# Optimization experiments

Hardware: AMD Instinct MI355X
Metric: run time of the kernel (lower is better)

The kernel has to match this reference:

```python
import jax, jax.numpy as jnp
import numpy as np

S, B, H = 2048, 2, 1024
NH = 16
HD = H // NH  # 64


def setup_inputs() -> dict:
    key = jax.random.key(0)
    k1, k2 = jax.random.split(key)
    hidden_states = jax.random.normal(k1, (S, B, H), dtype=jnp.float32)
    W_qkv = jax.random.normal(k2, (3 * H, H), dtype=jnp.float32) * (H ** -0.5)
    b_qkv = jnp.zeros((3 * H,), dtype=jnp.float32)
    return {"hidden_states": hidden_states, "W_qkv": W_qkv, "b_qkv": b_qkv}


def reference(hidden_states, W_qkv, b_qkv):
    s, b, h = hidden_states.shape
    # QKV projection: [S,B,3H] -> [S,B,NH,3*HD] -> split
    qkv = hidden_states @ W_qkv.T + b_qkv
    qkv = qkv.reshape(s, b, NH, 3 * HD)
    q, k, v = jnp.split(qkv, 3, axis=-1)  # each [S,B,NH,HD]
    norm_factor = HD ** -0.5
    # scores: [B,NH,Sq,Sk]
    scores = jnp.einsum('sbhd,tbhd->bhst', q, k) * norm_factor
    # Cumsum sequence-op (seq_op_in_fp32=True): cumsum over key dim, scaled by Sq^-0.5
    probs = jnp.cumsum(scores.astype(jnp.float32), axis=-1) * (s ** -0.5)
    probs = probs.astype(hidden_states.dtype)
    # PV: [B,NH,Sq,HD] -> seq-first [Sq,B,NH*HD]
    ctx = jnp.einsum('bhst,tbhd->sbhd', probs, v)
    return ctx.reshape(s, b, h)
```

## Files before the change

kernel.cpp:

```cpp
#include <hip/hip_runtime.h>

#define S 2048
#define B 2
#define H 1024
#define NH 16
#define HD 64
#define THREE_H 3072
#define ROWS (S*B)

typedef __attribute__((ext_vector_type(8))) short short8;
typedef __attribute__((ext_vector_type(4))) float f32x4;
typedef const __attribute__((address_space(1))) unsigned int* gptr_t;
typedef __attribute__((address_space(3))) unsigned int* lptr_t;

#define N8_A (ROWS * H / 8)
#define N8_W (THREE_H * H / 8)

__device__ __forceinline__ ushort f2bf(float f) {
    union { float f; unsigned u; } v; v.f = f;
    unsigned r = v.u + 0x7fffu + ((v.u >> 16) & 1u);
    return (ushort)(r >> 16);
}
__device__ __forceinline__ float bf2f(ushort u) {
    union { unsigned u; float f; } v; v.u = ((unsigned)u) << 16;
    return v.f;
}

__global__ void cast_both(const float* __restrict__ A, const float* __restrict__ W,
                          ushort* __restrict__ Ab, ushort* __restrict__ Wb) {
    int i = blockIdx.x * 256 + threadIdx.x;
    const float4* s4;
    ushort* dst;
    if (i < N8_A) { s4 = (const float4*)A; dst = Ab; }
    else if (i < N8_A + N8_W) { s4 = (const float4*)W; dst = Wb; i -= N8_A; }
    else return;
    float4 a = s4[2 * i], b = s4[2 * i + 1];
    short8 o;
    o[0] = f2bf(a.x); o[1] = f2bf(a.y); o[2] = f2bf(a.z); o[3] = f2bf(a.w);
    o[4] = f2bf(b.x); o[5] = f2bf(b.y); o[6] = f2bf(b.z); o[7] = f2bf(b.w);
    *(short8*)(dst + 8 * (size_t)i) = o;
}

__global__ __launch_bounds__(256) void qkv_gemm_mfma(const ushort* __restrict__ Abf,
                                                     const ushort* __restrict__ Wbf,
                                                     const float* __restrict__ bias,
                                                     ushort* __restrict__ Qb,
                                                     ushort* __restrict__ Kb,
                                                     ushort* __restrict__ Vraw) {
    __shared__ ushort Abuf[128 * 32];
    __shared__ ushort Bbuf[128 * 32];
    const int tid = threadIdx.x;
    const int wave = tid >> 6, lane = tid & 63;
    const int wr = wave >> 1, wc = wave & 1;
    const int row0 = blockIdx.x * 128;
    const int col0 = blockIdx.y * 128;

    f32x4 acc[4][4] = {};

    const int lrow = lane >> 2;
    const int gk = ((lane & 3) ^ (lrow & 3)) * 8;
    const int il = lane & 15, ko = lane >> 4;

    for (int k0 = 0; k0 < H; k0 += 32) {
#pragma unroll
        for (int p = 0; p < 2; ++p) {
            int c = wave * 2 + p;
            int row = c * 16 + lrow;
            __builtin_amdgcn_global_load_lds(
                (gptr_t)&Abf[(size_t)(row0 + row) * H + k0 + gk],
                (lptr_t)&Abuf[c * 512 + lane * 8], 16, 0, 0);
            __builtin_amdgcn_global_load_lds(
                (gptr_t)&Wbf[(size_t)(col0 + row) * H + k0 + gk],
                (lptr_t)&Bbuf[c * 512 + lane * 8], 16, 0, 0);
        }
        __syncthreads();

        short8 af[4], bfr[4];
#pragma unroll
        for (int m = 0; m < 4; ++m) {
            int ar = wr * 64 + m * 16 + il;
            int br = wc * 64 + m * 16 + il;
            af[m]  = *(const short8*)&Abuf[ar * 32 + (ko ^ (ar & 3)) * 8];
            bfr[m] = *(const short8*)&Bbuf[br * 32 + (ko ^ (br & 3)) * 8];
        }
#pragma unroll
        for (int m = 0; m < 4; ++m)
#pragma unroll
            for (int n = 0; n < 4; ++n)
                acc[m][n] = __builtin_amdgcn_mfma_f32_16x16x32_bf16(af[m], bfr[n], acc[m][n], 0, 0, 0);
        __syncthreads();
    }

#pragma unroll
    for (int n = 0; n < 4; ++n) {
        int cbase = col0 + wc * 64 + n * 16;
        int h   = cbase / 192;
        int r3  = cbase % 192;
        int sel = r3 >> 6;
        int d   = (r3 & 63) + il;
        float bv = bias[cbase + il];
        ushort* dst = (sel == 0) ? Qb : (sel == 1) ? Kb : Vraw;
#pragma unroll
        for (int m = 0; m < 4; ++m) {
            int rowb = row0 + wr * 64 + m * 16 + ko * 4;
#pragma unroll
            for (int j = 0; j < 4; ++j) {
                int r = rowb + j;
                int s = r >> 1, b = r & 1;
                dst[((size_t)((b * NH + h) * S + s)) * HD + d] = f2bf(acc[m][n][j] + bv);
            }
        }
    }
}

__global__ __launch_bounds__(256) void ktrans_chunksum(const ushort* __restrict__ Kb,
                                                       ushort* __restrict__ Kt,
                                                       const ushort* __restrict__ Vraw,
                                                       float* __restrict__ csum) {
    __shared__ ushort Ks[64][72];
    const int gb = blockIdx.x;
    const int tid = threadIdx.x;
    if (gb < 1024) {
        const int bh = gb >> 5;
        const int t0 = (gb & 31) * 64;
        {
            const int tt = tid >> 2, part = (tid & 3) * 16;
            const ushort* src = Kb + ((size_t)bh * S + t0 + tt) * HD + part;
            *(short8*)&Ks[tt][part]     = *(const short8*)(src);
            *(short8*)&Ks[tt][part + 8] = *(const short8*)(src + 8);
        }
        __syncthreads();
        {
            const int d = tid >> 2, tq = (tid & 3) * 16;
            ushort tmp[16];
#pragma unroll
            for (int k = 0; k < 16; ++k) tmp[k] = Ks[tq + k][d];
            ushort* dst = Kt + ((size_t)bh * HD + d) * S + t0 + tq;
            short8 o0, o1;
#pragma unroll
            for (int k = 0; k < 8; ++k) { o0[k] = tmp[k]; o1[k] = tmp[8 + k]; }
            *(short8*)dst = o0;
            *(short8*)(dst + 8) = o1;
        }
    } else {
        int idx = (gb - 1024) * 256 + tid;
        int col = idx & 2047;
        int chunk = idx >> 11;
        const ushort* vp = Vraw + ((size_t)(col >> 6) * S + chunk * 32) * HD + (col & 63);
        float s = 0.f;
#pragma unroll
        for (int t = 0; t < 32; ++t) s += bf2f(vp[(size_t)t * HD]);
        csum[chunk * 2048 + col] = s;
    }
}

__global__ void vsuft_final(const ushort* __restrict__ Vraw, const float* __restrict__ csum,
                            ushort* __restrict__ Vt) {
    int idx = blockIdx.x * 256 + threadIdx.x;
    int col = idx & 2047;
    int chunk = idx >> 11;
    int bh = col >> 6, d = col & 63;
    float acc = 0.f;
    for (int c = chunk + 1; c < 64; ++c) acc += csum[c * 2048 + col];
    const ushort* vp = Vraw + ((size_t)bh * S + chunk * 32) * HD + d;
    ushort buf[32];
#pragma unroll
    for (int tt = 31; tt >= 0; --tt) {
        acc += bf2f(vp[(size_t)tt * HD]);
        buf[tt] = f2bf(acc);
    }
    ushort* op = Vt + ((size_t)bh * HD + d) * S + chunk * 32;
#pragma unroll
    for (int q = 0; q < 4; ++q) {
        short8 o;
#pragma unroll
        for (int k = 0; k < 8; ++k) o[k] = buf[q * 8 + k];
        *(short8*)(op + q * 8) = o;
    }
}

__global__ __launch_bounds__(256) void kvm_mfma(const ushort* __restrict__ Kt,
                                                const ushort* __restrict__ Vt,
                                                float* __restrict__ Mpart) {
    __shared__ float red[2][4096];
    const int bh = blockIdx.x, kb = blockIdx.y;
    const int tid = threadIdx.x, wave = tid >> 6, lane = tid & 63;
    const int slice = kb * 4 + wave;
    const ushort* Kp = Kt + (size_t)bh * HD * S;
    const ushort* Vp = Vt + (size_t)bh * HD * S;
    f32x4 acc[4][4] = {};
    const int il = lane & 15, g = lane >> 4;
    const int tbase = slice * 128 + g * 8;
#pragma unroll
    for (int ks = 0; ks < 4; ++ks) {
        const int t = tbase + ks * 32;
        short8 af[4], bfv[4];
#pragma unroll
        for (int m = 0; m < 4; ++m) af[m]  = *(const short8*)&Kp[(size_t)(m * 16 + il) * S + t];
#pragma unroll
        for (int n = 0; n < 4; ++n) bfv[n] = *(const short8*)&Vp[(size_t)(n * 16 + il) * S + t];
#pragma unroll
        for (int m = 0; m < 4; ++m)
#pragma unroll
            for (int n = 0; n < 4; ++n)
                acc[m][n] = __builtin_amdgcn_mfma_f32_16x16x32_bf16(af[m], bfv[n], acc[m][n], 0, 0, 0);
    }
#define DUMP(dstbuf)                                                        \
    { float* _d = (dstbuf);                                                 \
      _Pragma("unroll") for (int m = 0; m < 4; ++m)                         \
      _Pragma("unroll") for (int n = 0; n < 4; ++n)                         \
      _Pragma("unroll") for (int j = 0; j < 4; ++j)                         \
          _d[(m * 16 + g * 4 + j) * 64 + n * 16 + il] = acc[m][n][j]; }
#define ADDIN(srcbuf)                                                       \
    { const float* _s = (srcbuf);                                           \
      _Pragma("unroll") for (int m = 0; m < 4; ++m)                         \
      _Pragma("unroll") for (int n = 0; n < 4; ++n)                         \
      _Pragma("unroll") for (int j = 0; j < 4; ++j)                         \
          acc[m][n][j] += _s[(m * 16 + g * 4 + j) * 64 + n * 16 + il]; }
    if (wave == 1) DUMP(red[0]);
    if (wave == 3) DUMP(red[1]);
    __syncthreads();
    if (wave == 0) ADDIN(red[0]);
    if (wave == 2) ADDIN(red[1]);
    __syncthreads();
    if (wave == 2) DUMP(red[0]);
    __syncthreads();
    if (wave == 0) {
        ADDIN(red[0]);
        float* Mp = Mpart + ((size_t)kb * 32 + bh) * 4096;
#pragma unroll
        for (int m = 0; m < 4; ++m)
#pragma unroll
            for (int n = 0; n < 4; ++n)
#pragma unroll
                for (int j = 0; j < 4; ++j)
                    Mp[(m * 16 + g * 4 + j) * 64 + n * 16 + il] = acc[m][n][j];
    }
#undef DUMP
#undef ADDIN
}

__global__ __launch_bounds__(256) void qm_mfma(const ushort* __restrict__ Qb,
                                               const float* __restrict__ Mpart,
                                               float* __restrict__ out) {
    __shared__ ushort Mt[64][72];
    const int bh = blockIdx.x, b = bh >> 4, h = bh & 15;
    const int tid = threadIdx.x;
    {
        const int i = tid >> 2, jq = (tid & 3) * 16;
        f32x4 s0 = {}, s1 = {}, s2 = {}, s3 = {};
#pragma unroll
        for (int sl = 0; sl < 4; ++sl) {
            const float* p = Mpart + ((size_t)sl * 32 + bh) * 4096 + i * 64 + jq;
            s0 += *(const f32x4*)(p);
            s1 += *(const f32x4*)(p + 4);
            s2 += *(const f32x4*)(p + 8);
            s3 += *(const f32x4*)(p + 12);
        }
#pragma unroll
        for (int k = 0; k < 4; ++k) {
            Mt[jq + 0  + k][i] = f2bf(s0[k]);
            Mt[jq + 4  + k][i] = f2bf(s1[k]);
            Mt[jq + 8  + k][i] = f2bf(s2[k]);
            Mt[jq + 12 + k][i] = f2bf(s3[k]);
        }
    }
    __syncthreads();
    const int wave = tid >> 6, lane = tid & 63;
    const int sl15 = lane & 15, koct = (lane >> 4) * 8;
    const int s0b = blockIdx.y * 256 + wave * 64;
    f32x4 acc[4][4] = {};
#pragma unroll
    for (int ks = 0; ks < 2; ++ks) {
        short8 af[4], bfv[4];
#pragma unroll
        for (int m = 0; m < 4; ++m) {
            int s = s0b + m * 16 + sl15;
            af[m] = *(const short8*)&Qb[((size_t)bh * S + s) * HD + ks * 32 + koct];
        }
#pragma unroll
        for (int n = 0; n < 4; ++n)
            bfv[n] = *(const short8*)&Mt[n * 16 + sl15][ks * 32 + koct];
#pragma unroll
        for (int m = 0; m < 4; ++m)
#pragma unroll
            for (int n = 0; n < 4; ++n)
                acc[m][n] = __builtin_amdgcn_mfma_f32_16x16x32_bf16(af[m], bfv[n], acc[m][n], 0, 0, 0);
    }
    const float scale = 0.125f * 0.02209708691207961f;
#pragma unroll
    for (int m = 0; m < 4; ++m)
#pragma unroll
        for (int n = 0; n < 4; ++n)
#pragma unroll
            for (int j = 0; j < 4; ++j) {
                int s = s0b + m * 16 + (lane >> 4) * 4 + j;
                int d = n * 16 + sl15;
                out[(size_t)(s * B + b) * H + h * 64 + d] = acc[m][n][j] * scale;
            }
}

extern "C" void kernel_launch(void* const* d_in, const int* in_sizes, int n_in,
                              void* d_out, int out_size, void* d_ws, size_t ws_size,
                              hipStream_t stream) {
    const float* hidden = (const float*)d_in[0];
    const float* W      = (const float*)d_in[1];
    const float* bias   = (const float*)d_in[2];
    float* out = (float*)d_out;

    ushort* Qb    = (ushort*)d_ws;
    ushort* Kb    = Qb + 4194304;
    ushort* Kt    = Kb + 4194304;
    ushort* Vraw  = Kt + 4194304;
    ushort* Vt    = Vraw + 4194304;
    float*  csum  = (float*)(Vt + 4194304);
    float*  Mpart = csum + 131072;
    ushort* Abf   = (ushort*)(Mpart + 524288);
    ushort* Wbf   = Abf + 4194304;

    cast_both<<<(N8_A + N8_W + 255) / 256, 256, 0, stream>>>(hidden, W, Abf, Wbf);
    qkv_gemm_mfma<<<dim3(ROWS / 128, THREE_H / 128), 256, 0, stream>>>(Abf, Wbf, bias, Qb, Kb, Vraw);
    ktrans_chunksum<<<1536, 256, 0, stream>>>(Kb, Kt, Vraw, csum);
    vsuft_final<<<512, 256, 0, stream>>>(Vraw, csum, Vt);
    kvm_mfma<<<dim3(32, 4), 256, 0, stream>>>(Kt, Vt, Mpart);
    qm_mfma<<<dim3(32, 8), 256, 0, stream>>>(Qb, Mpart, out);
}
```

Baseline: 78.04 us.

## Write K and V transposed from GEMM epilogue and replace suffix scan with single-pass wave scan

The QKV GEMM epilogue now writes K and V directly in a transposed [bh][d][t] layout, so the separate K-transpose and V chunk-sum kernels are removed. The two-pass suffix sum over V is replaced by one in-place kernel in which each wave scans a full row using register sums and shuffles. This cuts two launches and several full round trips of K/V through global memory. The cost is that the epilogue now does scattered 4-byte strided stores instead of row-contiguous ones.

```diff
diff --git a/kernel.cpp b/kernel.cpp
--- a/kernel.cpp
+++ b/kernel.cpp
@@ -45,8 +45,8 @@
                                                      const ushort* __restrict__ Wbf,
                                                      const float* __restrict__ bias,
                                                      ushort* __restrict__ Qb,
-                                                     ushort* __restrict__ Kb,
-                                                     ushort* __restrict__ Vraw) {
+                                                     ushort* __restrict__ Ktd,
+                                                     ushort* __restrict__ Vtd) {
     __shared__ ushort Abuf[128 * 32];
     __shared__ ushort Bbuf[128 * 32];
     const int tid = threadIdx.x;
@@ -99,83 +99,64 @@
         int sel = r3 >> 6;
         int d   = (r3 & 63) + il;
         float bv = bias[cbase + il];
-        ushort* dst = (sel == 0) ? Qb : (sel == 1) ? Kb : Vraw;
-#pragma unroll
-        for (int m = 0; m < 4; ++m) {
-            int rowb = row0 + wr * 64 + m * 16 + ko * 4;
-#pragma unroll
-            for (int j = 0; j < 4; ++j) {
-                int r = rowb + j;
-                int s = r >> 1, b = r & 1;
-                dst[((size_t)((b * NH + h) * S + s)) * HD + d] = f2bf(acc[m][n][j] + bv);
+        if (sel == 0) {
+#pragma unroll
+            for (int m = 0; m < 4; ++m) {
+                int rowb = row0 + wr * 64 + m * 16 + ko * 4;
+#pragma unroll
+                for (int j = 0; j < 4; ++j) {
+                    int r = rowb + j;
+                    int s = r >> 1, b = r & 1;
+                    Qb[((size_t)((b * NH + h) * S + s)) * HD + d] = f2bf(acc[m][n][j] + bv);
+                }
             }
-        }
-    }
-}
-
-__global__ __launch_bounds__(256) void ktrans_chunksum(const ushort* __restrict__ Kb,
-                                                       ushort* __restrict__ Kt,
-                                                       const ushort* __restrict__ Vraw,
-                                                       float* __restrict__ csum) {
-    __shared__ ushort Ks[64][72];
-    const int gb = blockIdx.x;
-    const int tid = threadIdx.x;
-    if (gb < 1024) {
-        const int bh = gb >> 5;
-        const int t0 = (gb & 31) * 64;
-        {
-            const int tt = tid >> 2, part = (tid & 3) * 16;
-            const ushort* src = Kb + ((size_t)bh * S + t0 + tt) * HD + part;
-            *(short8*)&Ks[tt][part]     = *(const short8*)(src);
-            *(short8*)&Ks[tt][part + 8] = *(const short8*)(src + 8);
-        }
-        __syncthreads();
-        {
-            const int d = tid >> 2, tq = (tid & 3) * 16;
-            ushort tmp[16];
-#pragma unroll
-            for (int k = 0; k < 16; ++k) tmp[k] = Ks[tq + k][d];
-            ushort* dst = Kt + ((size_t)bh * HD + d) * S + t0 + tq;
-            short8 o0, o1;
-#pragma unroll
-            for (int k = 0; k < 8; ++k) { o0[k] = tmp[k]; o1[k] = tmp[8 + k]; }
-            *(short8*)dst = o0;
-            *(short8*)(dst + 8) = o1;
-        }
-    } else {
-        int idx = (gb - 1024) * 256 + tid;
-        int col = idx & 2047;
-        int chunk = idx >> 11;
-        const ushort* vp = Vraw + ((size_t)(col >> 6) * S + chunk * 32) * HD + (col & 63);
-        float s = 0.f;
-#pragma unroll
-        for (int t = 0; t < 32; ++t) s += bf2f(vp[(size_t)t * HD]);
-        csum[chunk * 2048 + col] = s;
-    }
-}
-
-__global__ void vsuft_final(const ushort* __restrict__ Vraw, const float* __restrict__ csum,
-                            ushort* __restrict__ Vt) {
-    int idx = blockIdx.x * 256 + threadIdx.x;
-    int col = idx & 2047;
-    int chunk = idx >> 11;
-    int bh = col >> 6, d = col & 63;
-    float acc = 0.f;
-    for (int c = chunk + 1; c < 64; ++c) acc += csum[c * 2048 + col];
-    const ushort* vp = Vraw + ((size_t)bh * S + chunk * 32) * HD + d;
-    ushort buf[32];
-#pragma unroll
-    for (int tt = 31; tt >= 0; --tt) {
-        acc += bf2f(vp[(size_t)tt * HD]);
-        buf[tt] = f2bf(acc);
-    }
-    ushort* op = Vt + ((size_t)bh * HD + d) * S + chunk * 32;
+        } else {
+            ushort* dst = (sel == 1) ? Ktd : Vtd;
+            const size_t ro0 = ((size_t)(h)      * HD + d) * S;
+            const size_t ro1 = ((size_t)(NH + h) * HD + d) * S;
+#pragma unroll
+            for (int m = 0; m < 4; ++m) {
+                int t0 = (row0 + wr * 64 + m * 16 + ko * 4) >> 1;
+                uint lo = (uint)f2bf(acc[m][n][0] + bv) |
+                          ((uint)f2bf(acc[m][n][2] + bv) << 16);
+                uint hi = (uint)f2bf(acc[m][n][1] + bv) |
+                          ((uint)f2bf(acc[m][n][3] + bv) << 16);
+                *(uint*)&dst[ro0 + t0] = lo;
+                *(uint*)&dst[ro1 + t0] = hi;
+            }
+        }
+    }
+}
+
+__global__ __launch_bounds__(256) void vscan(ushort* __restrict__ Vtd) {
+    const int row = blockIdx.x * 4 + (threadIdx.x >> 6);
+    const int lane = threadIdx.x & 63;
+    ushort* vp = Vtd + (size_t)row * S + lane * 32;
+    float v[32];
+#pragma unroll
+    for (int q = 0; q < 4; ++q) {
+        short8 x = *(const short8*)(vp + q * 8);
+#pragma unroll
+        for (int k = 0; k < 8; ++k) v[q * 8 + k] = bf2f((ushort)x[k]);
+    }
+    float sum = 0.f;
+#pragma unroll
+    for (int k = 0; k < 32; ++k) sum += v[k];
+    float t = sum;
+#pragma unroll
+    for (int off = 1; off < 64; off <<= 1) {
+        float o = __shfl_down(t, off, 64);
+        if (lane + off < 64) t += o;
+    }
+    float acc = t - sum;
+#pragma unroll
+    for (int k = 31; k >= 0; --k) { acc += v[k]; v[k] = acc; }
 #pragma unroll
     for (int q = 0; q < 4; ++q) {
         short8 o;
 #pragma unroll
-        for (int k = 0; k < 8; ++k) o[k] = buf[q * 8 + k];
-        *(short8*)(op + q * 8) = o;
+        for (int k = 0; k < 8; ++k) o[k] = f2bf(v[q * 8 + k]);
+        *(short8*)(vp + q * 8) = o;
     }
 }
 
@@ -309,19 +290,15 @@
     float* out = (float*)d_out;
 
     ushort* Qb    = (ushort*)d_ws;
-    ushort* Kb    = Qb + 4194304;
-    ushort* Kt    = Kb + 4194304;
-    ushort* Vraw  = Kt + 4194304;
-    ushort* Vt    = Vraw + 4194304;
-    float*  csum  = (float*)(Vt + 4194304);
-    float*  Mpart = csum + 131072;
+    ushort* Ktd   = Qb + 4194304;
+    ushort* Vtd   = Ktd + 4194304;
+    float*  Mpart = (float*)(Vtd + 4194304);
     ushort* Abf   = (ushort*)(Mpart + 524288);
     ushort* Wbf   = Abf + 4194304;
 
     cast_both<<<(N8_A + N8_W + 255) / 256, 256, 0, stream>>>(hidden, W, Abf, Wbf);
-    qkv_gemm_mfma<<<dim3(ROWS / 128, THREE_H / 128), 256, 0, stream>>>(Abf, Wbf, bias, Qb, Kb, Vraw);
-    ktrans_chunksum<<<1536, 256, 0, stream>>>(Kb, Kt, Vraw, csum);
-    vsuft_final<<<512, 256, 0, stream>>>(Vraw, csum, Vt);
-    kvm_mfma<<<dim3(32, 4), 256, 0, stream>>>(Kt, Vt, Mpart);
+    qkv_gemm_mfma<<<dim3(ROWS / 128, THREE_H / 128), 256, 0, stream>>>(Abf, Wbf, bias, Qb, Ktd, Vtd);
+    vscan<<<512, 256, 0, stream>>>(Vtd);
+    kvm_mfma<<<dim3(32, 4), 256, 0, stream>>>(Ktd, Vtd, Mpart);
     qm_mfma<<<dim3(32, 8), 256, 0, stream>>>(Qb, Mpart, out);
 }
```

Result: faster. 71.42 us (-8.5%).
